# Kernel optimization log

Hardware: AMD Instinct MI355X
Metric: run time of the kernel (lower is better)

Reference implementation:

```python
import jax, jax.numpy as jnp
import numpy as np

N, D_IN, D_LAT, K = 200000, 256, 64, 100
ALPHA = 1000.0


def setup_inputs() -> dict:
    key = jax.random.key(0)
    k1, k2, k3, k4 = jax.random.split(key, 4)
    X = jax.random.normal(k1, (N, D_IN), dtype=jnp.float32)
    encoding = jax.random.normal(k2, (N, D_LAT), dtype=jnp.float32)
    decoding = jax.random.normal(k3, (N, D_IN), dtype=jnp.float32)
    # xavier_uniform bound for [K, D]: sqrt(6/(K+D))
    bound = np.sqrt(6.0 / (K + D_LAT)).astype(np.float32)
    centres = jax.random.uniform(k4, (K, D_LAT), dtype=jnp.float32,
                                 minval=-bound, maxval=bound)
    return {"X": X, "encoding": encoding, "decoding": decoding, "centres": centres}


def _cluster_kl(encoding, centres):
    # squared euclidean distances [N, K]
    d2 = (jnp.sum(encoding * encoding, axis=1, keepdims=True)
          + jnp.sum(centres * centres, axis=1)[None, :]
          - 2.0 * encoding @ centres.T)
    d2 = jnp.maximum(d2, 0.0)
    # Student-t (1 dof) soft assignment (DEC)
    q = 1.0 / (1.0 + d2)
    q = q / jnp.sum(q, axis=1, keepdims=True)          # [N, K]
    # target distribution p = (q^2 / f) normalized, detached
    f = jnp.sum(q, axis=0)                              # [K]
    p = (q * q) / f
    p = p / jnp.sum(p, axis=1, keepdims=True)
    p = jax.lax.stop_gradient(p)
    # F.kl_div(log q, p, reduction='batchmean') = sum p*(log p - log q) / N
    kl = jnp.sum(p * (jnp.log(p) - jnp.log(q))) / q.shape[0]
    return kl


def reference(X, encoding, decoding, centres):
    decoder_loss = jnp.mean((X - decoding) ** 2)
    cluster_loss = _cluster_kl(encoding, centres)
    return decoder_loss + cluster_loss * ALPHA
```

## Files before the change

kernel.cpp:

```cpp
#include <hip/hip_runtime.h>

#define N_ROWS 200000
#define D_IN   256
#define D_LAT  64
#define K_CL   100
#define NT     7
#define TPB    256

#define GRPS   3125
#define NMF    625
#define GPB    5

#define NS1    1563
#define NS2    1562
#define SPAIRS 16
#define BURST  8
#define SSTRIDE ((NS1 + NS2) * TPB)

#define NSLOT  64

typedef __attribute__((ext_vector_type(8))) short bf16x8;
typedef __attribute__((ext_vector_type(4))) float f32x4;

__device__ __forceinline__ float rcpf(float x) { return __builtin_amdgcn_rcpf(x); }

__device__ __forceinline__ short f2bf(float f) {
    union { float f; unsigned u; } v; v.f = f;
    unsigned r = (v.u + 0x7fffu + ((v.u >> 16) & 1u)) >> 16;
    return (short)r;
}

__device__ __forceinline__ void cvt8r(float4 a, float4 b, bf16x8& o, float& sq) {
    sq = fmaf(a.x, a.x, sq); sq = fmaf(a.y, a.y, sq);
    sq = fmaf(a.z, a.z, sq); sq = fmaf(a.w, a.w, sq);
    sq = fmaf(b.x, b.x, sq); sq = fmaf(b.y, b.y, sq);
    sq = fmaf(b.z, b.z, sq); sq = fmaf(b.w, b.w, sq);
    o[0] = f2bf(a.x); o[1] = f2bf(a.y); o[2] = f2bf(a.z); o[3] = f2bf(a.w);
    o[4] = f2bf(b.x); o[5] = f2bf(b.y); o[6] = f2bf(b.z); o[7] = f2bf(b.w);
}

__device__ __forceinline__ void cvt8(const float* __restrict__ p, bf16x8& o, float& sq) {
    float4 a = *(const float4*)p;
    float4 b = *(const float4*)(p + 4);
    cvt8r(a, b, o, sq);
}

#define LANE_IDS()                                                             \
    const int tid = threadIdx.x;                                               \
    const int l   = tid & 63;                                                  \
    const int w   = tid >> 6;                                                  \
    const int c16 = l & 15;                                                    \
    const int g   = l >> 4;

#define PROLOGUE_B()                                                           \
    bf16x8 bfrag[NT][2];                                                       \
    float  cn2v[NT];                                                           \
    _Pragma("unroll")                                                          \
    for (int t = 0; t < NT; ++t) {                                             \
        int col = t * 16 + c16;                                                \
        bool valid = col < K_CL;                                               \
        float sq = 0.f;                                                        \
        _Pragma("unroll")                                                      \
        for (int kt = 0; kt < 2; ++kt) {                                       \
            bf16x8 bf;                                                         \
            if (valid) {                                                       \
                cvt8(cen + col * D_LAT + kt * 32 + g * 8, bf, sq);             \
            } else {                                                           \
                _Pragma("unroll")                                              \
                for (int i = 0; i < 8; ++i) bf[i] = 0;                         \
            }                                                                  \
            bfrag[t][kt] = bf;                                                 \
        }                                                                      \
        sq += __shfl_xor(sq, 16);                                              \
        sq += __shfl_xor(sq, 32);                                              \
        cn2v[t] = sq;                                                          \
    }                                                                          \
    const bool v6 = (c16 < 4);

#define LOADS4(grp, A)                                                         \
    {                                                                          \
        const int rowbase_ = (grp) * 64 + w * 16;                              \
        const float* arow_ = enc + (size_t)(rowbase_ + c16) * D_LAT + g * 8;   \
        A[0] = *(const float4*)(arow_);                                        \
        A[1] = *(const float4*)(arow_ + 4);                                    \
        A[2] = *(const float4*)(arow_ + 32);                                   \
        A[3] = *(const float4*)(arow_ + 36);                                   \
    }

#define GROUP_COMPUTE_FROM(A)                                                  \
    float en2p = 0.f;                                                          \
    bf16x8 afrag0, afrag1;                                                     \
    cvt8r(A[0], A[1], afrag0, en2p);                                           \
    cvt8r(A[2], A[3], afrag1, en2p);                                           \
    en2p += __shfl_xor(en2p, 16);                                              \
    en2p += __shfl_xor(en2p, 32);                                              \
    f32x4 acc[NT];                                                             \
    _Pragma("unroll")                                                          \
    for (int t = 0; t < NT; ++t) {                                             \
        acc[t][0] = 0.f; acc[t][1] = 0.f; acc[t][2] = 0.f; acc[t][3] = 0.f;    \
    }                                                                          \
    _Pragma("unroll")                                                          \
    for (int t = 0; t < NT; ++t)                                               \
        acc[t] = __builtin_amdgcn_mfma_f32_16x16x32_bf16(afrag0, bfrag[t][0], acc[t], 0, 0, 0); \
    _Pragma("unroll")                                                          \
    for (int t = 0; t < NT; ++t)                                               \
        acc[t] = __builtin_amdgcn_mfma_f32_16x16x32_bf16(afrag1, bfrag[t][1], acc[t], 0, 0, 0); \
    float en2r[4];                                                             \
    _Pragma("unroll")                                                          \
    for (int r = 0; r < 4; ++r) en2r[r] = __shfl(en2p, g * 4 + r);             \
    float qv[NT][4];                                                           \
    float rs[4] = {0.f, 0.f, 0.f, 0.f};                                        \
    _Pragma("unroll")                                                          \
    for (int t = 0; t < NT; ++t) {                                             \
        _Pragma("unroll")                                                      \
        for (int r = 0; r < 4; ++r) {                                          \
            float d2 = en2r[r] + cn2v[t] - 2.f * acc[t][r];                    \
            float q = rcpf(1.f + fmaxf(d2, 0.f));                              \
            if (t == 6 && !v6) q = 0.f;                                        \
            qv[t][r] = q; rs[r] += q;                                          \
        }                                                                      \
    }                                                                          \
    _Pragma("unroll")                                                          \
    for (int r = 0; r < 4; ++r) {                                              \
        rs[r] += __shfl_xor(rs[r], 1); rs[r] += __shfl_xor(rs[r], 2);          \
        rs[r] += __shfl_xor(rs[r], 4); rs[r] += __shfl_xor(rs[r], 8);          \
        rs[r] = rcpf(rs[r]);                                                   \
    }

__device__ __forceinline__ void dec_stream(const f32x4* __restrict__ X,
                                           const f32x4* __restrict__ Dec,
                                           double* __restrict__ slots, int v) {
    int idx = v * TPB + (int)threadIdx.x;
    float local = 0.f;
#pragma unroll 1
    for (int o = 0; o < SPAIRS / BURST; ++o) {
        f32x4 a[BURST], b[BURST];
#pragma unroll
        for (int u = 0; u < BURST; ++u) {
            a[u] = __builtin_nontemporal_load(X + idx + u * SSTRIDE);
            b[u] = __builtin_nontemporal_load(Dec + idx + u * SSTRIDE);
        }
#pragma unroll
        for (int u = 0; u < BURST; ++u) {
            f32x4 d = a[u] - b[u];
            local = fmaf(d.x, d.x, local); local = fmaf(d.y, d.y, local);
            local = fmaf(d.z, d.z, local); local = fmaf(d.w, d.w, local);
        }
        idx += BURST * SSTRIDE;
    }
    __shared__ float red[TPB];
    red[threadIdx.x] = local;
    __syncthreads();
    for (int off = TPB / 2; off > 0; off >>= 1) {
        if (threadIdx.x < off) red[threadIdx.x] += red[threadIdx.x + off];
        __syncthreads();
    }
    if (threadIdx.x == 0) atomicAdd(&slots[v & (NSLOT - 1)], (double)red[0]);
}

__global__ void __launch_bounds__(TPB) k_d1(const f32x4* __restrict__ X,
                                            const f32x4* __restrict__ Xdec,
                                            const float* __restrict__ enc,
                                            const float* __restrict__ cen,
                                            double* __restrict__ dec_slots,
                                            float* __restrict__ fg) {
    if (blockIdx.x >= NMF) {
        dec_stream(X, Xdec, dec_slots, blockIdx.x - NMF);
        return;
    }
    LANE_IDS();
    const int p1id = blockIdx.x;
    float4 abuf[2][4];
    LOADS4(p1id, abuf[0]);
    PROLOGUE_B();
    float facc[NT];
#pragma unroll
    for (int t = 0; t < NT; ++t) facc[t] = 0.f;
#pragma unroll
    for (int j = 0; j < GPB; ++j) {
        if (j + 1 < GPB) LOADS4(p1id + (j + 1) * NMF, abuf[(j + 1) & 1]);
        GROUP_COMPUTE_FROM(abuf[j & 1]);
#pragma unroll
        for (int t = 0; t < NT; ++t) {
            float a = 0.f;
#pragma unroll
            for (int r = 0; r < 4; ++r) a = fmaf(qv[t][r], rs[r], a);
            facc[t] += a;
        }
    }
    __shared__ float f_s[K_CL];
    for (int i = tid; i < K_CL; i += TPB) f_s[i] = 0.f;
    __syncthreads();
#pragma unroll
    for (int t = 0; t < NT; ++t) {
        float a = facc[t];
        a += __shfl_xor(a, 16);
        a += __shfl_xor(a, 32);
        int col = t * 16 + c16;
        if (g == 0 && col < K_CL) atomicAdd(&f_s[col], a);
    }
    __syncthreads();
    for (int i = tid; i < K_CL; i += TPB) atomicAdd(&fg[i], f_s[i]);
}

__global__ void __launch_bounds__(TPB) k_d2(const f32x4* __restrict__ X,
                                            const f32x4* __restrict__ Xdec,
                                            const float* __restrict__ enc,
                                            const float* __restrict__ cen,
                                            const float* __restrict__ fg,
                                            double* __restrict__ dec_slots,
                                            double* __restrict__ kl_slots) {
    if (blockIdx.x >= NMF) {
        dec_stream(X, Xdec, dec_slots, NS1 + blockIdx.x - NMF);
        return;
    }
    LANE_IDS();
    const int p2id = blockIdx.x;
    float4 abuf[2][4];
    LOADS4(p2id, abuf[0]);
    PROLOGUE_B();
    float lfv[NT], rfv[NT];
#pragma unroll
    for (int t = 0; t < NT; ++t) {
        int col = t * 16 + c16;
        if (col < K_CL) {
            float fv = fg[col];
            lfv[t] = __logf(fv);
            rfv[t] = rcpf(fv);
        } else { lfv[t] = 0.f; rfv[t] = 0.f; }
    }
    float kl_local = 0.f;
#pragma unroll
    for (int j = 0; j < GPB; ++j) {
        if (j + 1 < GPB) LOADS4(p2id + (j + 1) * NMF, abuf[(j + 1) & 1]);
        GROUP_COMPUTE_FROM(abuf[j & 1]);
        float tac[4] = {0.f, 0.f, 0.f, 0.f};
        float Ap[4]  = {0.f, 0.f, 0.f, 0.f};
        float Bp[4]  = {0.f, 0.f, 0.f, 0.f};
#pragma unroll
        for (int t = 0; t < NT; ++t) {
#pragma unroll
            for (int r = 0; r < 4; ++r) {
                if (t == 6 && !v6) continue;
                float q = qv[t][r] * rs[r];
                float pu = q * q * rfv[t];
                tac[r] += pu;
                Ap[r] = fmaf(pu, __logf(q), Ap[r]);
                Bp[r] = fmaf(pu, lfv[t], Bp[r]);
            }
        }
#pragma unroll
        for (int r = 0; r < 4; ++r) {
            tac[r] += __shfl_xor(tac[r], 1); tac[r] += __shfl_xor(tac[r], 2);
            tac[r] += __shfl_xor(tac[r], 4); tac[r] += __shfl_xor(tac[r], 8);
            Ap[r]  += __shfl_xor(Ap[r], 1);  Ap[r]  += __shfl_xor(Ap[r], 2);
            Ap[r]  += __shfl_xor(Ap[r], 4);  Ap[r]  += __shfl_xor(Ap[r], 8);
            Bp[r]  += __shfl_xor(Bp[r], 1);  Bp[r]  += __shfl_xor(Bp[r], 2);
            Bp[r]  += __shfl_xor(Bp[r], 4);  Bp[r]  += __shfl_xor(Bp[r], 8);
        }
        if (c16 == 0) {
#pragma unroll
            for (int r = 0; r < 4; ++r)
                kl_local += (Ap[r] - Bp[r]) * rcpf(tac[r]) - __logf(tac[r]);
        }
    }
    __shared__ float red[TPB];
    red[tid] = kl_local;
    __syncthreads();
    for (int off = TPB / 2; off > 0; off >>= 1) {
        if (tid < off) red[tid] += red[tid + off];
        __syncthreads();
    }
    if (tid == 0) atomicAdd(&kl_slots[p2id & (NSLOT - 1)], (double)red[0]);
}

__global__ void k_final(const double* __restrict__ dec_s,
                        const double* __restrict__ kl_s,
                        float* __restrict__ out) {
    int l = threadIdx.x;
    double d = dec_s[l];
    double k = kl_s[l];
#pragma unroll
    for (int off = 32; off > 0; off >>= 1) {
        d += __shfl_xor(d, off);
        k += __shfl_xor(k, off);
    }
    if (l == 0)
        out[0] = (float)(d / ((double)N_ROWS * (double)D_IN) + 1000.0 * (k / (double)N_ROWS));
}

extern "C" void kernel_launch(void* const* d_in, const int* in_sizes, int n_in,
                              void* d_out, int out_size, void* d_ws, size_t ws_size,
                              hipStream_t stream) {
    (void)in_sizes; (void)n_in; (void)out_size; (void)ws_size;
    const float* X   = (const float*)d_in[0];
    const float* enc = (const float*)d_in[1];
    const float* dec = (const float*)d_in[2];
    const float* cen = (const float*)d_in[3];
    float* out = (float*)d_out;

    double* dec_slots = (double*)d_ws;
    double* kl_slots  = (double*)((char*)d_ws + 512);
    float*  fg        = (float*)((char*)d_ws + 1024);

    hipMemsetAsync(d_ws, 0, 1536, stream);
    k_d1<<<NMF + NS1, TPB, 0, stream>>>(
        (const f32x4*)X, (const f32x4*)dec, enc, cen, dec_slots, fg);
    k_d2<<<NMF + NS2, TPB, 0, stream>>>(
        (const f32x4*)X, (const f32x4*)dec, enc, cen, fg, dec_slots, kl_slots);
    k_final<<<1, 64, 0, stream>>>(dec_slots, kl_slots, out);
}
```

Before: 135.7 us.

## Stream decoder MSE with persistent grid-stride blocks over contiguous chunks

Replaces the one-shot decoder-loss streaming blocks (1563/1562 blocks, each loading 16 strided pairs) with 512 persistent blocks per kernel that loop over contiguous 2048-float4 chunks. Each block covers half of the data in a grid-stride pattern. A sched_barrier separates the batch of loads from the FMAs so all loads issue together. The aim is fewer blocks, less launch and reduction overhead, and more contiguous accesses, at the cost of less parallelism and possible load imbalance.

```diff
diff --git a/kernel.cpp b/kernel.cpp
--- a/kernel.cpp
+++ b/kernel.cpp
@@ -11,13 +11,10 @@
 #define NMF    625
 #define GPB    5
 
-#define NS1    1563
-#define NS2    1562
-#define SPAIRS 16
-#define BURST  8
-#define SSTRIDE ((NS1 + NS2) * TPB)
-
-#define NSLOT  64
+#define SCHUNKS   6250
+#define SC_HALF   3125
+#define NSTR      512
+#define NSLOT     64
 
 typedef __attribute__((ext_vector_type(8))) short bf16x8;
 typedef __attribute__((ext_vector_type(4))) float f32x4;
@@ -129,24 +126,26 @@
 
 __device__ __forceinline__ void dec_stream(const f32x4* __restrict__ X,
                                            const f32x4* __restrict__ Dec,
-                                           double* __restrict__ slots, int v) {
-    int idx = v * TPB + (int)threadIdx.x;
+                                           double* __restrict__ slots,
+                                           int sid, int cbase) {
     float local = 0.f;
 #pragma unroll 1
-    for (int o = 0; o < SPAIRS / BURST; ++o) {
-        f32x4 a[BURST], b[BURST];
-#pragma unroll
-        for (int u = 0; u < BURST; ++u) {
-            a[u] = __builtin_nontemporal_load(X + idx + u * SSTRIDE);
-            b[u] = __builtin_nontemporal_load(Dec + idx + u * SSTRIDE);
-        }
-#pragma unroll
-        for (int u = 0; u < BURST; ++u) {
+    for (int c = sid; c < SC_HALF; c += NSTR) {
+        const int idx = (cbase + c) * 2048 + (int)threadIdx.x;
+        f32x4 a[8], b[8];
+#pragma unroll
+        for (int u = 0; u < 8; ++u)
+            a[u] = __builtin_nontemporal_load(X + idx + u * 256);
+#pragma unroll
+        for (int u = 0; u < 8; ++u)
+            b[u] = __builtin_nontemporal_load(Dec + idx + u * 256);
+        __builtin_amdgcn_sched_barrier(0);
+#pragma unroll
+        for (int u = 0; u < 8; ++u) {
             f32x4 d = a[u] - b[u];
             local = fmaf(d.x, d.x, local); local = fmaf(d.y, d.y, local);
             local = fmaf(d.z, d.z, local); local = fmaf(d.w, d.w, local);
         }
-        idx += BURST * SSTRIDE;
     }
     __shared__ float red[TPB];
     red[threadIdx.x] = local;
@@ -155,7 +154,7 @@
         if (threadIdx.x < off) red[threadIdx.x] += red[threadIdx.x + off];
         __syncthreads();
     }
-    if (threadIdx.x == 0) atomicAdd(&slots[v & (NSLOT - 1)], (double)red[0]);
+    if (threadIdx.x == 0) atomicAdd(&slots[sid & (NSLOT - 1)], (double)red[0]);
 }
 
 __global__ void __launch_bounds__(TPB) k_d1(const f32x4* __restrict__ X,
@@ -165,7 +164,7 @@
                                             double* __restrict__ dec_slots,
                                             float* __restrict__ fg) {
     if (blockIdx.x >= NMF) {
-        dec_stream(X, Xdec, dec_slots, blockIdx.x - NMF);
+        dec_stream(X, Xdec, dec_slots, blockIdx.x - NMF, 0);
         return;
     }
     LANE_IDS();
@@ -211,7 +210,7 @@
                                             double* __restrict__ dec_slots,
                                             double* __restrict__ kl_slots) {
     if (blockIdx.x >= NMF) {
-        dec_stream(X, Xdec, dec_slots, NS1 + blockIdx.x - NMF);
+        dec_stream(X, Xdec, dec_slots, blockIdx.x - NMF, SC_HALF);
         return;
     }
     LANE_IDS();
@@ -304,9 +303,9 @@
     float*  fg        = (float*)((char*)d_ws + 1024);
 
     hipMemsetAsync(d_ws, 0, 1536, stream);
-    k_d1<<<NMF + NS1, TPB, 0, stream>>>(
+    k_d1<<<NMF + NSTR, TPB, 0, stream>>>(
         (const f32x4*)X, (const f32x4*)dec, enc, cen, dec_slots, fg);
-    k_d2<<<NMF + NS2, TPB, 0, stream>>>(
+    k_d2<<<NMF + NSTR, TPB, 0, stream>>>(
         (const f32x4*)X, (const f32x4*)dec, enc, cen, fg, dec_slots, kl_slots);
     k_final<<<1, 64, 0, stream>>>(dec_slots, kl_slots, out);
 }
```

After: 133.9 us. About the same (-1.3%).
